# Performance work log

Hardware: AMD Instinct MI355X
Metric: run time of the kernel (lower is better)

Reference implementation:

```python
import jax, jax.numpy as jnp
import numpy as np

K = 2            # top-k experts
TEMP = 1.0       # temperature
LN_EPS = 1e-5

def setup_inputs() -> dict:
    key = jax.random.key(0)
    B, S, D, E = 4, 4096, 2048, 64
    k0, k1, k2, k3 = jax.random.split(key, 4)
    x = jax.random.normal(k0, (B, S, D), dtype=jnp.float32)
    Wg = jax.random.normal(k1, (E, D), dtype=jnp.float32) * 0.02       # base_gate weight [out,in]
    gamma = jnp.ones((D,), jnp.float32)                                 # LayerNorm weight
    beta = jnp.zeros((D,), jnp.float32)                                 # LayerNorm bias
    W1 = jax.random.normal(k2, (D // 2, D), dtype=jnp.float32) * 0.02   # diff_pred linear1
    W2 = jax.random.normal(k3, (1, D // 2), dtype=jnp.float32) * 0.02   # diff_pred linear2
    return {"x": x, "Wg": Wg, "gamma": gamma, "beta": beta, "W1": W1, "W2": W2}

def reference(x, Wg, gamma, beta, W1, W2):
    # base expert logits: [B,S,E]
    logits = jnp.einsum('bsd,ed->bse', x, Wg)
    # difficulty predictor: LN -> Linear -> GELU -> Linear -> sigmoid, [B,S,1]
    mu = jnp.mean(x, axis=-1, keepdims=True)
    var = jnp.var(x, axis=-1, keepdims=True)
    h = (x - mu) * jax.lax.rsqrt(var + LN_EPS) * gamma + beta
    h1 = jax.nn.gelu(jnp.einsum('bsd,hd->bsh', h, W1), approximate=False)
    diff = jax.nn.sigmoid(jnp.einsum('bsh,oh->bso', h1, W2))
    # modulate + temperature (eval mode: no jitter / mask_drop)
    logits = logits / (1.0 + diff) * (1.0 / TEMP)
    probs_soft = jax.nn.softmax(logits, axis=-1)
    # top-k selection
    _, idx = jax.lax.top_k(logits, K)                    # [B,S,K]
    hard_any = jnp.max(jax.nn.one_hot(idx, logits.shape[-1], dtype=probs_soft.dtype), axis=2)  # [B,S,E]
    probs_st = hard_any - probs_soft + probs_soft        # faithful to source (no detach)
    scores = jnp.take_along_axis(probs_st, idx, axis=-1)  # [B,S,K]
    scores = scores / jnp.maximum(jnp.sum(scores, axis=-1, keepdims=True), 1e-9)
    importance = jax.lax.stop_gradient(jnp.mean(probs_soft, axis=(0, 1)))  # [E]
    load = jax.lax.stop_gradient(jnp.mean(hard_any, axis=(0, 1)))          # [E]
    return (idx, scores, probs_soft, importance, load)
```

## Files before the change

### kernel.cpp

```cpp
#include <hip/hip_runtime.h>
#include <math.h>

#define BS_TOK 16384
#define DIM    2048
#define NEXP   64
#define DHID   1024
#define GKS    4
#define KSL    (DIM / GKS)

typedef __attribute__((ext_vector_type(8))) _Float16 f16x8;
typedef __attribute__((ext_vector_type(4))) float    f32x4;

#define GLOBAL_AS const __attribute__((address_space(1))) void*
#define LDS_AS    __attribute__((address_space(3))) void*

__device__ __forceinline__ float gelu_f(float x) {
  return 0.5f * x * (1.0f + erff(x * 0.70710678118654752440f));
}

__global__ __launch_bounds__(256) void ln_kernel(const float* __restrict__ X,
                                                 const float* __restrict__ gamma,
                                                 const float* __restrict__ beta,
                                                 _Float16* __restrict__ H) {
  const int tid  = threadIdx.x;
  const int w    = tid >> 6, lane = tid & 63;
  const int t    = blockIdx.x * 4 + w;
  const float* xr = X + (size_t)t * DIM;
  float4 xv[8];
#pragma unroll
  for (int j = 0; j < 4; ++j) {
    const int c0 = (j * 64 + lane) * 8;
    xv[j * 2]     = *(const float4*)(xr + c0);
    xv[j * 2 + 1] = *(const float4*)(xr + c0 + 4);
  }
  float s = 0.f, q = 0.f;
#pragma unroll
  for (int j = 0; j < 8; ++j) {
    s += (xv[j].x + xv[j].y) + (xv[j].z + xv[j].w);
    q += (xv[j].x * xv[j].x + xv[j].y * xv[j].y) + (xv[j].z * xv[j].z + xv[j].w * xv[j].w);
  }
#pragma unroll
  for (int off = 32; off > 0; off >>= 1) {
    s += __shfl_xor(s, off);
    q += __shfl_xor(q, off);
  }
  const float mu  = s * (1.0f / DIM);
  const float var = q * (1.0f / DIM) - mu * mu;
  const float rs  = rsqrtf(var + 1e-5f);
#pragma unroll
  for (int j = 0; j < 4; ++j) {
    const int c0 = (j * 64 + lane) * 8;
    const float4 g0 = *(const float4*)(gamma + c0);
    const float4 g1 = *(const float4*)(gamma + c0 + 4);
    const float4 b0 = *(const float4*)(beta + c0);
    const float4 b1 = *(const float4*)(beta + c0 + 4);
    const float4 a = xv[j * 2], b = xv[j * 2 + 1];
    f16x8 h;
    h[0] = (_Float16)((a.x - mu) * rs * g0.x + b0.x);
    h[1] = (_Float16)((a.y - mu) * rs * g0.y + b0.y);
    h[2] = (_Float16)((a.z - mu) * rs * g0.z + b0.z);
    h[3] = (_Float16)((a.w - mu) * rs * g0.w + b0.w);
    h[4] = (_Float16)((b.x - mu) * rs * g1.x + b1.x);
    h[5] = (_Float16)((b.y - mu) * rs * g1.y + b1.y);
    h[6] = (_Float16)((b.z - mu) * rs * g1.z + b1.z);
    h[7] = (_Float16)((b.w - mu) * rs * g1.w + b1.w);
    *(f16x8*)(H + (size_t)t * DIM + c0) = h;
  }
}

__global__ __launch_bounds__(256) void w1cast_kernel(const float* __restrict__ W1,
                                                     _Float16* __restrict__ W1h) {
  const int i = (blockIdx.x * 256 + threadIdx.x) * 8;
  const float4 a = *(const float4*)(W1 + i);
  const float4 b = *(const float4*)(W1 + i + 4);
  f16x8 o;
  o[0] = (_Float16)a.x; o[1] = (_Float16)a.y; o[2] = (_Float16)a.z; o[3] = (_Float16)a.w;
  o[4] = (_Float16)b.x; o[5] = (_Float16)b.y; o[6] = (_Float16)b.z; o[7] = (_Float16)b.w;
  *(f16x8*)(W1h + i) = o;
}

#define GT_M 256
#define PX   260
#define PW   68
__global__ __launch_bounds__(256) void gate_kernel(const float* __restrict__ X,
                                                   const float* __restrict__ Wg,
                                                   float* __restrict__ logitsP) {
  __shared__ float sX[16][PX];
  __shared__ float sW[16][PW];
  const int tid  = threadIdx.x;
  const int m0   = blockIdx.x * GT_M;
  const int k0   = blockIdx.y * KSL;
  const int srow = tid >> 2;
  const int skq  = tid & 3;
  const int ty   = tid >> 3;
  const int tx   = tid & 7;
  const float* xb = X  + (size_t)(m0 + srow) * DIM + k0 + skq * 4;
  const float* wb = Wg + (size_t)srow * DIM + k0 + skq * 4;
  float acc[8][8] = {};
  float4 rx[4], rw;
#pragma unroll
  for (int g = 0; g < 4; ++g) rx[g] = *(const float4*)(xb + (size_t)(g * 64) * DIM);
  rw = *(const float4*)wb;
  for (int kt = 0; kt < KSL; kt += 16) {
    __syncthreads();
#pragma unroll
    for (int g = 0; g < 4; ++g) {
      sX[skq * 4 + 0][srow + g * 64] = rx[g].x;
      sX[skq * 4 + 1][srow + g * 64] = rx[g].y;
      sX[skq * 4 + 2][srow + g * 64] = rx[g].z;
      sX[skq * 4 + 3][srow + g * 64] = rx[g].w;
    }
    sW[skq * 4 + 0][srow] = rw.x;
    sW[skq * 4 + 1][srow] = rw.y;
    sW[skq * 4 + 2][srow] = rw.z;
    sW[skq * 4 + 3][srow] = rw.w;
    const int ktn = (kt + 16 < KSL) ? kt + 16 : 0;
#pragma unroll
    for (int g = 0; g < 4; ++g) rx[g] = *(const float4*)(xb + (size_t)(g * 64) * DIM + ktn);
    rw = *(const float4*)(wb + ktn);
    __syncthreads();
#pragma unroll
    for (int k = 0; k < 16; ++k) {
      const float4 a0 = *(const float4*)&sX[k][ty * 8];
      const float4 a1 = *(const float4*)&sX[k][ty * 8 + 4];
      const float4 b0 = *(const float4*)&sW[k][tx * 8];
      const float4 b1 = *(const float4*)&sW[k][tx * 8 + 4];
      const float av[8] = {a0.x, a0.y, a0.z, a0.w, a1.x, a1.y, a1.z, a1.w};
      const float bv[8] = {b0.x, b0.y, b0.z, b0.w, b1.x, b1.y, b1.z, b1.w};
#pragma unroll
      for (int i = 0; i < 8; ++i)
#pragma unroll
        for (int j = 0; j < 8; ++j) acc[i][j] += av[i] * bv[j];
    }
  }
  float* op = logitsP + (size_t)blockIdx.y * ((size_t)BS_TOK * NEXP)
            + (size_t)(m0 + ty * 8) * NEXP + tx * 8;
#pragma unroll
  for (int i = 0; i < 8; ++i) {
    float4 o0, o1;
    o0.x = acc[i][0]; o0.y = acc[i][1]; o0.z = acc[i][2]; o0.w = acc[i][3];
    o1.x = acc[i][4]; o1.y = acc[i][5]; o1.z = acc[i][6]; o1.w = acc[i][7];
    *(float4*)(op + (size_t)i * NEXP)     = o0;
    *(float4*)(op + (size_t)i * NEXP + 4) = o1;
  }
}

#define G2BM 256
#define G2BN 256
#define G2BK 64
#define G2NT (DIM / G2BK)

__global__ __launch_bounds__(512, 2) void g2_kernel(const _Float16* __restrict__ H,
                                                    const _Float16* __restrict__ W1h,
                                                    const float* __restrict__ W2,
                                                    float* __restrict__ diffz) {
  __shared__ __align__(16) _Float16 sA[2][G2BM * G2BK];
  __shared__ __align__(16) _Float16 sB[2][G2BN * G2BK];
  const int bid = blockIdx.x;
  const int xcd = bid & 7;
  const int loc = bid >> 3;
  const int m0  = (xcd * 8 + (loc >> 2)) * G2BM;
  const int n0  = (loc & 3) * G2BN;
  const int tid  = threadIdx.x;
  const int lane = tid & 63;
  const int w    = tid >> 6;
  const int wr   = w >> 2, wc = w & 3;
  const int col  = lane & 15, quad = lane >> 4;
  const int c0   = col & 7;
  const int srow8 = tid >> 3;
  const int ksw   = (tid & 7) ^ (srow8 & 7);
  const _Float16* gA = H   + (size_t)(m0 + srow8) * DIM + ksw * 8;
  const _Float16* gB = W1h + (size_t)(n0 + srow8) * DIM + ksw * 8;
  f32x4 acc[8][4] = {};
#define G2_STAGE(bf_, kt_)                                                                          \
  do {                                                                                              \
    __builtin_amdgcn_global_load_lds((GLOBAL_AS)(gA + (kt_)),                 (LDS_AS)(sA[bf_] + tid * 8), 16, 0, 0);          \
    __builtin_amdgcn_global_load_lds((GLOBAL_AS)(gA + (size_t)64  * DIM + (kt_)), (LDS_AS)(sA[bf_] + 4096 + tid * 8), 16, 0, 0);   \
    __builtin_amdgcn_global_load_lds((GLOBAL_AS)(gA + (size_t)128 * DIM + (kt_)), (LDS_AS)(sA[bf_] + 8192 + tid * 8), 16, 0, 0);   \
    __builtin_amdgcn_global_load_lds((GLOBAL_AS)(gA + (size_t)192 * DIM + (kt_)), (LDS_AS)(sA[bf_] + 12288 + tid * 8), 16, 0, 0);  \
    __builtin_amdgcn_global_load_lds((GLOBAL_AS)(gB + (kt_)),                 (LDS_AS)(sB[bf_] + tid * 8), 16, 0, 0);          \
    __builtin_amdgcn_global_load_lds((GLOBAL_AS)(gB + (size_t)64  * DIM + (kt_)), (LDS_AS)(sB[bf_] + 4096 + tid * 8), 16, 0, 0);   \
    __builtin_amdgcn_global_load_lds((GLOBAL_AS)(gB + (size_t)128 * DIM + (kt_)), (LDS_AS)(sB[bf_] + 8192 + tid * 8), 16, 0, 0);   \
    __builtin_amdgcn_global_load_lds((GLOBAL_AS)(gB + (size_t)192 * DIM + (kt_)), (LDS_AS)(sB[bf_] + 12288 + tid * 8), 16, 0, 0);  \
  } while (0)
  G2_STAGE(0, 0);
  asm volatile("s_waitcnt vmcnt(0)" ::: "memory");
  __builtin_amdgcn_s_barrier();
  int cur = 0;
  for (int t = 0; t < G2NT; ++t) {
    if (t + 1 < G2NT) G2_STAGE(cur ^ 1, (t + 1) * G2BK);
    const _Float16* A = sA[cur];
    const _Float16* B = sB[cur];
    f16x8 af[4], bfr[4];
#pragma unroll
    for (int kh = 0; kh < 2; ++kh) {
      const int sqz = ((kh * 4 + quad) ^ c0) * 8;
#pragma unroll
      for (int ni = 0; ni < 4; ++ni)
        bfr[ni] = *(const f16x8*)(B + (wc * 64 + ni * 16 + col) * G2BK + sqz);
#pragma unroll
      for (int mi = 0; mi < 4; ++mi)
        af[mi] = *(const f16x8*)(A + (wr * 128 + mi * 16 + col) * G2BK + sqz);
      __builtin_amdgcn_s_setprio(1);
#pragma unroll
      for (int mi = 0; mi < 4; ++mi)
#pragma unroll
        for (int ni = 0; ni < 4; ++ni)
          acc[mi][ni] = __builtin_amdgcn_mfma_f32_16x16x32_f16(af[mi], bfr[ni], acc[mi][ni], 0, 0, 0);
      __builtin_amdgcn_s_setprio(0);
      __builtin_amdgcn_s_barrier();
#pragma unroll
      for (int mi = 0; mi < 4; ++mi)
        af[mi] = *(const f16x8*)(A + (wr * 128 + (mi + 4) * 16 + col) * G2BK + sqz);
      __builtin_amdgcn_s_setprio(1);
#pragma unroll
      for (int mi = 0; mi < 4; ++mi)
#pragma unroll
        for (int ni = 0; ni < 4; ++ni)
          acc[mi + 4][ni] = __builtin_amdgcn_mfma_f32_16x16x32_f16(af[mi], bfr[ni], acc[mi + 4][ni], 0, 0, 0);
      __builtin_amdgcn_s_setprio(0);
      __builtin_amdgcn_s_barrier();
    }
    if (t + 1 < G2NT) asm volatile("s_waitcnt vmcnt(0)" ::: "memory");
    __builtin_amdgcn_s_barrier();
    cur ^= 1;
  }
#undef G2_STAGE
  float w2v[4];
#pragma unroll
  for (int ni = 0; ni < 4; ++ni) w2v[ni] = W2[n0 + wc * 64 + ni * 16 + col];
#pragma unroll
  for (int mi = 0; mi < 8; ++mi) {
#pragma unroll
    for (int reg = 0; reg < 4; ++reg) {
      float v = 0.f;
#pragma unroll
      for (int ni = 0; ni < 4; ++ni) v += gelu_f(acc[mi][ni][reg]) * w2v[ni];
      v += __shfl_xor(v, 1);
      v += __shfl_xor(v, 2);
      v += __shfl_xor(v, 4);
      v += __shfl_xor(v, 8);
      if (col == 0)
        atomicAdd(diffz + m0 + wr * 128 + mi * 16 + quad * 4 + reg, v);
    }
  }
}

__global__ __launch_bounds__(256) void finalize_kernel(const float* __restrict__ logitsP,
                                                       const float* __restrict__ diffz,
                                                       float* __restrict__ out_idx,
                                                       float* __restrict__ out_scores,
                                                       float* __restrict__ out_probs,
                                                       float* __restrict__ imp_acc,
                                                       float* __restrict__ load_acc) {
  const int tid  = threadIdx.x;
  const int w    = tid >> 6, lane = tid & 63;
  const size_t PS = (size_t)BS_TOK * NEXP;
  float acc_imp = 0.f, acc_load = 0.f;
  for (int it = 0; it < 8; ++it) {
    const int t    = blockIdx.x * 32 + it * 4 + w;
    const float* lp = logitsP + (size_t)t * NEXP + lane;
    const float L  = ((lp[0] + lp[PS]) + lp[2 * PS]) + lp[3 * PS];
    const float z  = diffz[t];
    const float d  = 1.0f / (1.0f + expf(-z));
    const float l  = L / (1.0f + d);
    float m = l;
#pragma unroll
    for (int off = 32; off > 0; off >>= 1) m = fmaxf(m, __shfl_xor(m, off));
    float p = expf(l - m);
    float s = p;
#pragma unroll
    for (int off = 32; off > 0; off >>= 1) s += __shfl_xor(s, off);
    p /= s;
    float v = l; int bi = lane;
#pragma unroll
    for (int off = 32; off > 0; off >>= 1) {
      const float ov = __shfl_xor(v, off);
      const int   oi = __shfl_xor(bi, off);
      if (ov > v || (ov == v && oi < bi)) { v = ov; bi = oi; }
    }
    const int i1 = bi;
    float v2 = (lane == i1) ? -INFINITY : l;
    int bi2 = lane;
#pragma unroll
    for (int off = 32; off > 0; off >>= 1) {
      const float ov = __shfl_xor(v2, off);
      const int   oi = __shfl_xor(bi2, off);
      if (ov > v2 || (ov == v2 && oi < bi2)) { v2 = ov; bi2 = oi; }
    }
    const int i2 = bi2;
    const float p1 = __shfl(p, i1);
    const float p2 = __shfl(p, i2);
    const float s1 = (1.0f - p1) + p1;
    const float s2 = (1.0f - p2) + p2;
    const float den = fmaxf(s1 + s2, 1e-9f);
    if (lane == 0) {
      out_idx[t * 2]        = (float)i1;
      out_idx[t * 2 + 1]    = (float)i2;
      out_scores[t * 2]     = s1 / den;
      out_scores[t * 2 + 1] = s2 / den;
    }
    out_probs[(size_t)t * NEXP + lane] = p;
    acc_imp  += p;
    acc_load += (lane == i1 || lane == i2) ? 1.0f : 0.0f;
  }
  __shared__ float s_imp[256];
  __shared__ float s_hard[256];
  s_imp[tid]  = acc_imp;
  s_hard[tid] = acc_load;
  __syncthreads();
  if (tid < 64) {
    const float si = s_imp[tid] + s_imp[64 + tid] + s_imp[128 + tid] + s_imp[192 + tid];
    const float sl = s_hard[tid] + s_hard[64 + tid] + s_hard[128 + tid] + s_hard[192 + tid];
    atomicAdd(imp_acc + tid, si);
    atomicAdd(load_acc + tid, sl);
  }
}

__global__ void scale_kernel(const float* __restrict__ acc,
                             float* __restrict__ out_imp,
                             float* __restrict__ out_load) {
  const int tid = threadIdx.x;
  const float inv = 1.0f / 16384.0f;
  if (tid < 64)       out_imp[tid]        = acc[tid] * inv;
  else if (tid < 128) out_load[tid - 64]  = acc[tid] * inv;
}

extern "C" void kernel_launch(void* const* d_in, const int* in_sizes, int n_in,
                              void* d_out, int out_size, void* d_ws, size_t ws_size,
                              hipStream_t stream) {
  (void)in_sizes; (void)n_in; (void)out_size; (void)ws_size;
  const float* X     = (const float*)d_in[0];
  const float* Wg    = (const float*)d_in[1];
  const float* gamma = (const float*)d_in[2];
  const float* beta  = (const float*)d_in[3];
  const float* W1    = (const float*)d_in[4];
  const float* W2    = (const float*)d_in[5];
  float* out = (float*)d_out;

  char* ws = (char*)d_ws;
  _Float16* H       = (_Float16*)(ws);
  _Float16* W1h     = (_Float16*)(ws + 67108864ull);
  float*    logitsP = (float*)  (ws + 71303168ull);
  float*    diffz   = (float*)  (ws + 88080384ull);
  float*    accs    = (float*)  (ws + 88145920ull);

  float* out_idx    = out;
  float* out_scores = out + 32768;
  float* out_probs  = out + 65536;
  float* out_imp    = out + 1114112;
  float* out_load   = out + 1114176;

  hipMemsetAsync(diffz, 0, 65536ull + 512ull, stream);
  gate_kernel<<<dim3(BS_TOK / GT_M, GKS), 256, 0, stream>>>(X, Wg, logitsP);
  ln_kernel<<<BS_TOK / 4, 256, 0, stream>>>(X, gamma, beta, H);
  w1cast_kernel<<<(DHID * DIM) / (256 * 8), 256, 0, stream>>>(W1, W1h);
  g2_kernel<<<(DHID / G2BN) * (BS_TOK / G2BM), 512, 0, stream>>>(H, W1h, W2, diffz);
  finalize_kernel<<<BS_TOK / 32, 256, 0, stream>>>(logitsP, diffz, out_idx, out_scores,
                                                   out_probs, accs, accs + 64);
  scale_kernel<<<1, 128, 0, stream>>>(accs, out_imp, out_load);
}
```

Measured before the change: 366.7 us.

## Triple-buffer g2 GEMM with BK=32, merge LN/W1 cast and fold scale into finalize

```diff
diff --git a/kernel.cpp b/kernel.cpp
--- a/kernel.cpp
+++ b/kernel.cpp
@@ -18,11 +18,23 @@
   return 0.5f * x * (1.0f + erff(x * 0.70710678118654752440f));
 }
 
-__global__ __launch_bounds__(256) void ln_kernel(const float* __restrict__ X,
-                                                 const float* __restrict__ gamma,
-                                                 const float* __restrict__ beta,
-                                                 _Float16* __restrict__ H) {
-  const int tid  = threadIdx.x;
+__global__ __launch_bounds__(256) void lnw1_kernel(const float* __restrict__ X,
+                                                   const float* __restrict__ gamma,
+                                                   const float* __restrict__ beta,
+                                                   _Float16* __restrict__ H,
+                                                   const float* __restrict__ W1,
+                                                   _Float16* __restrict__ W1h) {
+  const int tid = threadIdx.x;
+  if (blockIdx.x >= BS_TOK / 4) {
+    const int i = ((blockIdx.x - BS_TOK / 4) * 256 + tid) * 8;
+    const float4 a = *(const float4*)(W1 + i);
+    const float4 b = *(const float4*)(W1 + i + 4);
+    f16x8 o;
+    o[0] = (_Float16)a.x; o[1] = (_Float16)a.y; o[2] = (_Float16)a.z; o[3] = (_Float16)a.w;
+    o[4] = (_Float16)b.x; o[5] = (_Float16)b.y; o[6] = (_Float16)b.z; o[7] = (_Float16)b.w;
+    *(f16x8*)(W1h + i) = o;
+    return;
+  }
   const int w    = tid >> 6, lane = tid & 63;
   const int t    = blockIdx.x * 4 + w;
   const float* xr = X + (size_t)t * DIM;
@@ -66,17 +78,6 @@
     h[7] = (_Float16)((b.w - mu) * rs * g1.w + b1.w);
     *(f16x8*)(H + (size_t)t * DIM + c0) = h;
   }
-}
-
-__global__ __launch_bounds__(256) void w1cast_kernel(const float* __restrict__ W1,
-                                                     _Float16* __restrict__ W1h) {
-  const int i = (blockIdx.x * 256 + threadIdx.x) * 8;
-  const float4 a = *(const float4*)(W1 + i);
-  const float4 b = *(const float4*)(W1 + i + 4);
-  f16x8 o;
-  o[0] = (_Float16)a.x; o[1] = (_Float16)a.y; o[2] = (_Float16)a.z; o[3] = (_Float16)a.w;
-  o[4] = (_Float16)b.x; o[5] = (_Float16)b.y; o[6] = (_Float16)b.z; o[7] = (_Float16)b.w;
-  *(f16x8*)(W1h + i) = o;
 }
 
 #define GT_M 256
@@ -147,15 +148,15 @@
 
 #define G2BM 256
 #define G2BN 256
-#define G2BK 64
+#define G2BK 32
 #define G2NT (DIM / G2BK)
 
 __global__ __launch_bounds__(512, 2) void g2_kernel(const _Float16* __restrict__ H,
                                                     const _Float16* __restrict__ W1h,
                                                     const float* __restrict__ W2,
                                                     float* __restrict__ diffz) {
-  __shared__ __align__(16) _Float16 sA[2][G2BM * G2BK];
-  __shared__ __align__(16) _Float16 sB[2][G2BN * G2BK];
+  __shared__ __align__(16) _Float16 sA[3][G2BM * G2BK];
+  __shared__ __align__(16) _Float16 sB[3][G2BN * G2BK];
   const int bid = blockIdx.x;
   const int xcd = bid & 7;
   const int loc = bid >> 3;
@@ -166,64 +167,60 @@
   const int w    = tid >> 6;
   const int wr   = w >> 2, wc = w & 3;
   const int col  = lane & 15, quad = lane >> 4;
-  const int c0   = col & 7;
-  const int srow8 = tid >> 3;
-  const int ksw   = (tid & 7) ^ (srow8 & 7);
-  const _Float16* gA = H   + (size_t)(m0 + srow8) * DIM + ksw * 8;
-  const _Float16* gB = W1h + (size_t)(n0 + srow8) * DIM + ksw * 8;
+  const int sq   = (quad ^ (col & 3)) * 8;
+  const int srow4 = tid >> 2;
+  const int ksw   = (tid & 3) ^ (srow4 & 3);
+  const _Float16* gA = H   + (size_t)(m0 + srow4) * DIM + ksw * 8;
+  const _Float16* gB = W1h + (size_t)(n0 + srow4) * DIM + ksw * 8;
   f32x4 acc[8][4] = {};
-#define G2_STAGE(bf_, kt_)                                                                          \
-  do {                                                                                              \
-    __builtin_amdgcn_global_load_lds((GLOBAL_AS)(gA + (kt_)),                 (LDS_AS)(sA[bf_] + tid * 8), 16, 0, 0);          \
-    __builtin_amdgcn_global_load_lds((GLOBAL_AS)(gA + (size_t)64  * DIM + (kt_)), (LDS_AS)(sA[bf_] + 4096 + tid * 8), 16, 0, 0);   \
-    __builtin_amdgcn_global_load_lds((GLOBAL_AS)(gA + (size_t)128 * DIM + (kt_)), (LDS_AS)(sA[bf_] + 8192 + tid * 8), 16, 0, 0);   \
-    __builtin_amdgcn_global_load_lds((GLOBAL_AS)(gA + (size_t)192 * DIM + (kt_)), (LDS_AS)(sA[bf_] + 12288 + tid * 8), 16, 0, 0);  \
-    __builtin_amdgcn_global_load_lds((GLOBAL_AS)(gB + (kt_)),                 (LDS_AS)(sB[bf_] + tid * 8), 16, 0, 0);          \
-    __builtin_amdgcn_global_load_lds((GLOBAL_AS)(gB + (size_t)64  * DIM + (kt_)), (LDS_AS)(sB[bf_] + 4096 + tid * 8), 16, 0, 0);   \
-    __builtin_amdgcn_global_load_lds((GLOBAL_AS)(gB + (size_t)128 * DIM + (kt_)), (LDS_AS)(sB[bf_] + 8192 + tid * 8), 16, 0, 0);   \
-    __builtin_amdgcn_global_load_lds((GLOBAL_AS)(gB + (size_t)192 * DIM + (kt_)), (LDS_AS)(sB[bf_] + 12288 + tid * 8), 16, 0, 0);  \
+#define G2_STAGE(bf_, kt_) do {                                                                             \
+    __builtin_amdgcn_global_load_lds((GLOBAL_AS)(gA + (kt_)), (LDS_AS)(sA[bf_] + tid * 8), 16, 0, 0);        \
+    __builtin_amdgcn_global_load_lds((GLOBAL_AS)(gA + (size_t)128 * DIM + (kt_)), (LDS_AS)(sA[bf_] + 4096 + tid * 8), 16, 0, 0); \
+    __builtin_amdgcn_global_load_lds((GLOBAL_AS)(gB + (kt_)), (LDS_AS)(sB[bf_] + tid * 8), 16, 0, 0);        \
+    __builtin_amdgcn_global_load_lds((GLOBAL_AS)(gB + (size_t)128 * DIM + (kt_)), (LDS_AS)(sB[bf_] + 4096 + tid * 8), 16, 0, 0); \
   } while (0)
   G2_STAGE(0, 0);
-  asm volatile("s_waitcnt vmcnt(0)" ::: "memory");
+  G2_STAGE(1, G2BK);
+  asm volatile("s_waitcnt vmcnt(4)" ::: "memory");
   __builtin_amdgcn_s_barrier();
   int cur = 0;
   for (int t = 0; t < G2NT; ++t) {
-    if (t + 1 < G2NT) G2_STAGE(cur ^ 1, (t + 1) * G2BK);
     const _Float16* A = sA[cur];
     const _Float16* B = sB[cur];
+    const int nb = (cur >= 1) ? cur - 1 : 2;
+    if (t + 2 < G2NT) G2_STAGE(nb, (t + 2) * G2BK);
     f16x8 af[4], bfr[4];
 #pragma unroll
-    for (int kh = 0; kh < 2; ++kh) {
-      const int sqz = ((kh * 4 + quad) ^ c0) * 8;
+    for (int ni = 0; ni < 4; ++ni)
+      bfr[ni] = *(const f16x8*)(B + (wc * 64 + ni * 16 + col) * G2BK + sq);
+#pragma unroll
+    for (int mi = 0; mi < 4; ++mi)
+      af[mi] = *(const f16x8*)(A + (wr * 128 + mi * 16 + col) * G2BK + sq);
+    __builtin_amdgcn_s_barrier();
+    __builtin_amdgcn_s_setprio(1);
+#pragma unroll
+    for (int mi = 0; mi < 4; ++mi)
 #pragma unroll
       for (int ni = 0; ni < 4; ++ni)
-        bfr[ni] = *(const f16x8*)(B + (wc * 64 + ni * 16 + col) * G2BK + sqz);
-#pragma unroll
-      for (int mi = 0; mi < 4; ++mi)
-        af[mi] = *(const f16x8*)(A + (wr * 128 + mi * 16 + col) * G2BK + sqz);
-      __builtin_amdgcn_s_setprio(1);
-#pragma unroll
-      for (int mi = 0; mi < 4; ++mi)
-#pragma unroll
-        for (int ni = 0; ni < 4; ++ni)
-          acc[mi][ni] = __builtin_amdgcn_mfma_f32_16x16x32_f16(af[mi], bfr[ni], acc[mi][ni], 0, 0, 0);
-      __builtin_amdgcn_s_setprio(0);
-      __builtin_amdgcn_s_barrier();
-#pragma unroll
-      for (int mi = 0; mi < 4; ++mi)
-        af[mi] = *(const f16x8*)(A + (wr * 128 + (mi + 4) * 16 + col) * G2BK + sqz);
-      __builtin_amdgcn_s_setprio(1);
-#pragma unroll
-      for (int mi = 0; mi < 4; ++mi)
-#pragma unroll
-        for (int ni = 0; ni < 4; ++ni)
-          acc[mi + 4][ni] = __builtin_amdgcn_mfma_f32_16x16x32_f16(af[mi], bfr[ni], acc[mi + 4][ni], 0, 0, 0);
-      __builtin_amdgcn_s_setprio(0);
-      __builtin_amdgcn_s_barrier();
-    }
-    if (t + 1 < G2NT) asm volatile("s_waitcnt vmcnt(0)" ::: "memory");
+        acc[mi][ni] = __builtin_amdgcn_mfma_f32_16x16x32_f16(af[mi], bfr[ni], acc[mi][ni], 0, 0, 0);
+    __builtin_amdgcn_s_setprio(0);
     __builtin_amdgcn_s_barrier();
-    cur ^= 1;
+#pragma unroll
+    for (int mi = 0; mi < 4; ++mi)
+      af[mi] = *(const f16x8*)(A + (wr * 128 + (mi + 4) * 16 + col) * G2BK + sq);
+    __builtin_amdgcn_s_barrier();
+    __builtin_amdgcn_s_setprio(1);
+#pragma unroll
+    for (int mi = 0; mi < 4; ++mi)
+#pragma unroll
+      for (int ni = 0; ni < 4; ++ni)
+        acc[mi + 4][ni] = __builtin_amdgcn_mfma_f32_16x16x32_f16(af[mi], bfr[ni], acc[mi + 4][ni], 0, 0, 0);
+    __builtin_amdgcn_s_setprio(0);
+    if (t + 2 < G2NT) asm volatile("s_waitcnt vmcnt(4) lgkmcnt(0)" ::: "memory");
+    else              asm volatile("s_waitcnt vmcnt(0) lgkmcnt(0)" ::: "memory");
+    __builtin_amdgcn_sched_barrier(0);
+    __builtin_amdgcn_s_barrier();
+    cur = (cur == 2) ? 0 : cur + 1;
   }
 #undef G2_STAGE
   float w2v[4];
@@ -251,8 +248,9 @@
                                                        float* __restrict__ out_idx,
                                                        float* __restrict__ out_scores,
                                                        float* __restrict__ out_probs,
-                                                       float* __restrict__ imp_acc,
-                                                       float* __restrict__ load_acc) {
+                                                       float* __restrict__ accs,
+                                                       float* __restrict__ out_imp,
+                                                       float* __restrict__ out_load) {
   const int tid  = threadIdx.x;
   const int w    = tid >> 6, lane = tid & 63;
   const size_t PS = (size_t)BS_TOK * NEXP;
@@ -312,18 +310,23 @@
   if (tid < 64) {
     const float si = s_imp[tid] + s_imp[64 + tid] + s_imp[128 + tid] + s_imp[192 + tid];
     const float sl = s_hard[tid] + s_hard[64 + tid] + s_hard[128 + tid] + s_hard[192 + tid];
-    atomicAdd(imp_acc + tid, si);
-    atomicAdd(load_acc + tid, sl);
-  }
-}
-
-__global__ void scale_kernel(const float* __restrict__ acc,
-                             float* __restrict__ out_imp,
-                             float* __restrict__ out_load) {
-  const int tid = threadIdx.x;
-  const float inv = 1.0f / 16384.0f;
-  if (tid < 64)       out_imp[tid]        = acc[tid] * inv;
-  else if (tid < 128) out_load[tid - 64]  = acc[tid] * inv;
+    atomicAdd(accs + tid, si);
+    atomicAdd(accs + 64 + tid, sl);
+    __threadfence();
+  }
+  __shared__ int lastf;
+  __syncthreads();
+  if (tid == 0) {
+    unsigned* cnt = (unsigned*)(accs + 128);
+    lastf = (atomicAdd(cnt, 1u) == (unsigned)(BS_TOK / 32) - 1u);
+  }
+  __syncthreads();
+  if (lastf && tid < 128) {
+    const float v = atomicAdd(accs + tid, 0.0f);
+    const float inv = 1.0f / 16384.0f;
+    if (tid < 64) out_imp[tid]       = v * inv;
+    else          out_load[tid - 64] = v * inv;
+  }
 }
 
 extern "C" void kernel_launch(void* const* d_in, const int* in_sizes, int n_in,
@@ -351,12 +354,10 @@
   float* out_imp    = out + 1114112;
   float* out_load   = out + 1114176;
 
-  hipMemsetAsync(diffz, 0, 65536ull + 512ull, stream);
+  hipMemsetAsync(diffz, 0, 66560ull, stream);
   gate_kernel<<<dim3(BS_TOK / GT_M, GKS), 256, 0, stream>>>(X, Wg, logitsP);
-  ln_kernel<<<BS_TOK / 4, 256, 0, stream>>>(X, gamma, beta, H);
-  w1cast_kernel<<<(DHID * DIM) / (256 * 8), 256, 0, stream>>>(W1, W1h);
+  lnw1_kernel<<<BS_TOK / 4 + (DHID * DIM) / (256 * 8), 256, 0, stream>>>(X, gamma, beta, H, W1, W1h);
   g2_kernel<<<(DHID / G2BN) * (BS_TOK / G2BM), 512, 0, stream>>>(H, W1h, W2, diffz);
   finalize_kernel<<<BS_TOK / 32, 256, 0, stream>>>(logitsP, diffz, out_idx, out_scores,
-                                                   out_probs, accs, accs + 64);
-  scale_kernel<<<1, 128, 0, stream>>>(accs, out_imp, out_load);
-}
+                                                   out_probs, accs, out_imp, out_load);
+}
```

After: 391.5 us. 1.07x slower.
